# Optimization experiments

Hardware: AMD Instinct MI355X
Metric: run time of the kernel (lower is better)

## Reference

```python
import jax, jax.numpy as jnp
import numpy as np

N, B, S, F_DIM, E = 100000, 4096, 32, 256, 256


def _linear_params(key, fan_in, fan_out):
    kw, kb = jax.random.split(key)
    bound = 1.0 / np.sqrt(fan_in)
    W = jax.random.uniform(kw, (fan_in, fan_out), jnp.float32, -bound, bound)
    b = jax.random.uniform(kb, (fan_out,), jnp.float32, -bound, bound)
    return W, b


def setup_inputs() -> dict:
    key = jax.random.key(0)
    ks = jax.random.split(key, 10)
    Wm, bm = _linear_params(ks[4], F_DIM, E)
    Wq, bq = _linear_params(ks[5], F_DIM, E)
    Wk, bk = _linear_params(ks[6], F_DIM, E)
    Wv, bv = _linear_params(ks[7], F_DIM, E)
    Wc, bc = _linear_params(ks[8], 2 * E, E)
    return {
        "nodes": jax.random.randint(ks[0], (B,), 0, N),
        "neigh_mean": jax.random.randint(ks[1], (B, S), 0, N),
        "neigh_attn": jax.random.randint(ks[2], (B, S), 0, N),
        "id2feat": jax.random.normal(ks[3], (N, F_DIM), jnp.float32),
        "Wm": Wm, "bm": bm,
        "Wq": Wq, "bq": bq,
        "Wk": Wk, "bk": bk,
        "Wv": Wv, "bv": bv,
        "Wc": Wc, "bc": bc,
    }


def reference(nodes, neigh_mean, neigh_attn, id2feat,
              Wm, bm, Wq, bq, Wk, bk, Wv, bv, Wc, bc):
    self_feats = id2feat[nodes]                                   # [B, F]

    # MeanAggregator1: per-row mean of W(id2feat[neighbors]).
    # (mean(W x + b) == W mean(x) + b by linearity; all rows have S neighbors)
    ctx = jnp.mean(id2feat[neigh_mean], axis=1) @ Wm + bm          # [B, E]

    # AttnAggregator1: self-query attention over [neighbors ; self].
    neigh = id2feat[neigh_attn]                                    # [B, S, F]
    cat = jnp.concatenate([neigh, self_feats[:, None, :]], axis=1)  # [B, S+1, F]
    Q = self_feats @ Wq + bq                                       # [B, E]
    K = cat @ Wk + bk                                              # [B, S+1, E]
    V = cat @ Wv + bv                                              # [B, S+1, E]
    scores = jnp.einsum('be,bse->bs', Q, K)                        # [B, S+1]
    # Torch mask loop with uniform neighbor length S masks column S (the self slot)
    pad_mask = jnp.arange(S + 1) >= S                              # [S+1]
    scores = jnp.where(pad_mask[None, :], -jnp.inf, scores)
    attn = jax.nn.softmax(scores, axis=-1)
    mix = jnp.einsum('bs,bse->be', attn, V)                        # [B, E]

    combined = jnp.tanh(jnp.concatenate([mix, ctx], axis=-1) @ Wc + bc)  # [B, E]
    norm = jnp.linalg.norm(combined, axis=-1, keepdims=True)
    return combined / jnp.maximum(norm, 1e-12)                     # F.normalize(p=2)
```

## Files before the change

### kernel.cpp

```cpp
#include <hip/hip_runtime.h>
#include <math.h>

#define S_NEI 32

__global__ __launch_bounds__(256) void transpose256(const float* __restrict__ in,
                                                    float* __restrict__ outT) {
    __shared__ float tile[32][33];
    const int bx = blockIdx.x * 32, by = blockIdx.y * 32;
    const int x = threadIdx.x, y = threadIdx.y;
#pragma unroll
    for (int i = 0; i < 32; i += 8)
        tile[y + i][x] = in[(by + y + i) * 256 + bx + x];
    __syncthreads();
#pragma unroll
    for (int i = 0; i < 32; i += 8)
        outT[(bx + y + i) * 256 + by + x] = tile[x][y + i];
}

template <int KT>
__device__ __forceinline__ void gemm_tile8(const float* __restrict__ A, int row0,
                                           const float* __restrict__ B,
                                           float acc[2][4], float* __restrict__ sA,
                                           float* __restrict__ sB) {
    const int t = threadIdx.x;
    const int tr = t >> 6, tc = t & 63;
    const int r = t >> 5;
    const int k1 = t & 31;
    const size_t arow = (size_t)(row0 + r) * KT;
    for (int kb = 0; kb < KT; kb += 32) {
        sA[k1 * 12 + r] = A[arow + kb + k1];
#pragma unroll
        for (int i = 0; i < 8; ++i) {
            *reinterpret_cast<float4*>(&sB[(i * 4 + tr) * 256 + tc * 4]) =
                *reinterpret_cast<const float4*>(&B[(size_t)(kb + i * 4 + tr) * 256 + tc * 4]);
        }
        __syncthreads();
#pragma unroll
        for (int k = 0; k < 32; ++k) {
            const float2 a2 = *reinterpret_cast<const float2*>(&sA[k * 12 + tr * 2]);
            const float4 b4 = *reinterpret_cast<const float4*>(&sB[k * 256 + tc * 4]);
            acc[0][0] += a2.x * b4.x; acc[0][1] += a2.x * b4.y;
            acc[0][2] += a2.x * b4.z; acc[0][3] += a2.x * b4.w;
            acc[1][0] += a2.y * b4.x; acc[1][1] += a2.y * b4.y;
            acc[1][2] += a2.y * b4.z; acc[1][3] += a2.y * b4.w;
        }
        __syncthreads();
    }
}

__global__ __launch_bounds__(256) void precompute3(const float* __restrict__ Wq,
                                                   const float* __restrict__ Wv,
                                                   const float* __restrict__ Wm,
                                                   const float* __restrict__ Wc,
                                                   const float* __restrict__ WkT,
                                                   float* __restrict__ Wqk,
                                                   float* __restrict__ Wvc,
                                                   float* __restrict__ Wmc) {
    __shared__ float sA[32 * 12];
    __shared__ float sB[32 * 256];
    float acc[2][4] = {};
    const float *Ap, *Bp;
    float* Cp;
    switch (blockIdx.y) {
        case 0: Ap = Wq; Bp = WkT; Cp = Wqk; break;
        case 1: Ap = Wv; Bp = Wc; Cp = Wvc; break;
        default: Ap = Wm; Bp = Wc + 256 * 256; Cp = Wmc; break;
    }
    const int row0 = blockIdx.x * 8;
    gemm_tile8<256>(Ap, row0, Bp, acc, sA, sB);
    const int tr = threadIdx.x >> 6, tc = threadIdx.x & 63;
#pragma unroll
    for (int i = 0; i < 2; ++i) {
        float4 v = make_float4(acc[i][0], acc[i][1], acc[i][2], acc[i][3]);
        *reinterpret_cast<float4*>(&Cp[(row0 + tr * 2 + i) * 256 + tc * 4]) = v;
    }
}

__global__ __launch_bounds__(256) void bias_k(const float* __restrict__ bq,
                                              const float* __restrict__ bv,
                                              const float* __restrict__ bm,
                                              const float* __restrict__ bc,
                                              const float* __restrict__ Wc,
                                              const float* __restrict__ WkT,
                                              float* __restrict__ bqk,
                                              float* __restrict__ bfull) {
    const int c = blockIdx.x;
    const int e = threadIdx.x;
    const int w = e >> 6, l = e & 63;
    float a = bq[e] * WkT[e * 256 + c];
    float v = bv[e] * Wc[e * 256 + c] + bm[e] * Wc[(256 + e) * 256 + c];
    __shared__ float redA[4], redV[4];
#pragma unroll
    for (int off = 32; off; off >>= 1) { a += __shfl_xor(a, off); v += __shfl_xor(v, off); }
    if (l == 0) { redA[w] = a; redV[w] = v; }
    __syncthreads();
    if (e == 0) {
        bqk[c] = redA[0] + redA[1] + redA[2] + redA[3];
        bfull[c] = bc[c] + redV[0] + redV[1] + redV[2] + redV[3];
    }
}

#define FMA8(a0, a1, b4)                                                   \
    do {                                                                   \
        acc[0][0] += (a0).x * (b4).x; acc[0][1] += (a0).x * (b4).y;        \
        acc[0][2] += (a0).x * (b4).z; acc[0][3] += (a0).x * (b4).w;        \
        acc[1][0] += (a0).y * (b4).x; acc[1][1] += (a0).y * (b4).y;        \
        acc[1][2] += (a0).y * (b4).z; acc[1][3] += (a0).y * (b4).w;        \
        acc[2][0] += (a0).z * (b4).x; acc[2][1] += (a0).z * (b4).y;        \
        acc[2][2] += (a0).z * (b4).z; acc[2][3] += (a0).z * (b4).w;        \
        acc[3][0] += (a0).w * (b4).x; acc[3][1] += (a0).w * (b4).y;        \
        acc[3][2] += (a0).w * (b4).z; acc[3][3] += (a0).w * (b4).w;        \
        acc[4][0] += (a1).x * (b4).x; acc[4][1] += (a1).x * (b4).y;        \
        acc[4][2] += (a1).x * (b4).z; acc[4][3] += (a1).x * (b4).w;        \
        acc[5][0] += (a1).y * (b4).x; acc[5][1] += (a1).y * (b4).y;        \
        acc[5][2] += (a1).y * (b4).z; acc[5][3] += (a1).y * (b4).w;        \
        acc[6][0] += (a1).z * (b4).x; acc[6][1] += (a1).z * (b4).y;        \
        acc[6][2] += (a1).z * (b4).z; acc[6][3] += (a1).z * (b4).w;        \
        acc[7][0] += (a1).w * (b4).x; acc[7][1] += (a1).w * (b4).y;        \
        acc[7][2] += (a1).w * (b4).z; acc[7][3] += (a1).w * (b4).w;        \
    } while (0)

__global__ __launch_bounds__(256, 2) void fused8(const float* __restrict__ id2feat,
                                                 const int* __restrict__ nodes,
                                                 const int* __restrict__ neigh_mean,
                                                 const int* __restrict__ neigh_attn,
                                                 const float* __restrict__ Wqk,
                                                 const float* __restrict__ bqk,
                                                 const float* __restrict__ Wfused,
                                                 const float* __restrict__ bfull,
                                                 float* __restrict__ out) {
    __shared__ __align__(16) char smem[59904];
    float* sA  = (float*)smem;
    float* sAF = (float*)smem;
    float* sP  = (float*)(smem + 24576);
    float* sQk = (float*)(smem + 49536);
    int*   sIA = (int*)(smem + 57856);
    int*   sIM = (int*)(smem + 58880);

    const int t = threadIdx.x;
    const int w = t >> 6, l = t & 63;
    const int col4 = l * 4;
    const int row0 = blockIdx.x * 8;

    sIA[t] = neigh_attn[(size_t)row0 * S_NEI + t];
    sIM[t] = neigh_mean[(size_t)row0 * S_NEI + t];

    {
        const int r = t & 7;
        const int k0 = (t >> 3) * 8;
        const size_t arow = (size_t)nodes[row0 + r] * 256;
#pragma unroll
        for (int u = 0; u < 2; ++u) {
            const float4 v = *reinterpret_cast<const float4*>(&id2feat[arow + k0 + u * 4]);
            sA[(k0 + u * 4 + 0) * 12 + r] = v.x;
            sA[(k0 + u * 4 + 1) * 12 + r] = v.y;
            sA[(k0 + u * 4 + 2) * 12 + r] = v.z;
            sA[(k0 + u * 4 + 3) * 12 + r] = v.w;
        }
    }
    __syncthreads();

    float acc[8][4] = {};

    {
        const int kbeg = w * 64;
        const float* Bp = Wqk + (size_t)kbeg * 256 + col4;
        float4 bufA[8], bufB[8];
#pragma unroll
        for (int j = 0; j < 8; ++j)
            bufA[j] = *reinterpret_cast<const float4*>(&Bp[(size_t)j * 256]);
        for (int kb = 0; kb < 64; kb += 16) {
#pragma unroll
            for (int j = 0; j < 8; ++j)
                bufB[j] = *reinterpret_cast<const float4*>(&Bp[(size_t)(kb + 8 + j) * 256]);
#pragma unroll
            for (int j = 0; j < 8; ++j) {
                const int k = kbeg + kb + j;
                const float4 a0 = *reinterpret_cast<const float4*>(&sA[k * 12]);
                const float4 a1 = *reinterpret_cast<const float4*>(&sA[k * 12 + 4]);
                FMA8(a0, a1, bufA[j]);
            }
            if (kb + 16 < 64) {
#pragma unroll
                for (int j = 0; j < 8; ++j)
                    bufA[j] = *reinterpret_cast<const float4*>(&Bp[(size_t)(kb + 16 + j) * 256]);
            }
#pragma unroll
            for (int j = 0; j < 8; ++j) {
                const int k = kbeg + kb + 8 + j;
                const float4 a0 = *reinterpret_cast<const float4*>(&sA[k * 12]);
                const float4 a1 = *reinterpret_cast<const float4*>(&sA[k * 12 + 4]);
                FMA8(a0, a1, bufB[j]);
            }
        }
    }
    if (w > 0) {
#pragma unroll
        for (int i = 0; i < 8; ++i)
            *reinterpret_cast<float4*>(&sP[(w - 1) * 2080 + i * 260 + col4]) =
                make_float4(acc[i][0], acc[i][1], acc[i][2], acc[i][3]);
    }
    __syncthreads();
    if (w == 0) {
        const float4 bq4 = *reinterpret_cast<const float4*>(&bqk[col4]);
#pragma unroll
        for (int i = 0; i < 8; ++i) {
            float4 v = make_float4(acc[i][0] + bq4.x, acc[i][1] + bq4.y,
                                   acc[i][2] + bq4.z, acc[i][3] + bq4.w);
#pragma unroll
            for (int pw = 0; pw < 3; ++pw) {
                const float4 p =
                    *reinterpret_cast<const float4*>(&sP[pw * 2080 + i * 260 + col4]);
                v.x += p.x; v.y += p.y; v.z += p.z; v.w += p.w;
            }
            *reinterpret_cast<float4*>(&sQk[i * 260 + col4]) = v;
        }
    }
    __syncthreads();

    const float4* f4 = reinterpret_cast<const float4*>(id2feat);
#pragma unroll
    for (int bb = 0; bb < 2; ++bb) {
        const int b = w * 2 + bb;
        float4 r[32];
#pragma unroll
        for (int j = 0; j < 32; ++j) r[j] = f4[(size_t)sIA[b * 32 + j] * 64 + l];
        float4 macc = make_float4(0.f, 0.f, 0.f, 0.f);
#pragma unroll
        for (int j = 0; j < 32; ++j) {
            const float4 v = f4[(size_t)sIM[b * 32 + j] * 64 + l];
            macc.x += v.x; macc.y += v.y; macc.z += v.z; macc.w += v.w;
        }
        const float4 q = *reinterpret_cast<const float4*>(&sQk[b * 260 + col4]);
        float sc[32];
#pragma unroll
        for (int j = 0; j < 32; ++j) {
            float p = q.x * r[j].x + q.y * r[j].y + q.z * r[j].z + q.w * r[j].w;
#pragma unroll
            for (int off = 32; off; off >>= 1) p += __shfl_xor(p, off);
            sc[j] = p;
        }
        float m = sc[0];
#pragma unroll
        for (int j = 1; j < 32; ++j) m = fmaxf(m, sc[j]);
        float sum = 0.f;
#pragma unroll
        for (int j = 0; j < 32; ++j) sum += __expf(sc[j] - m);
        const float inv = 1.0f / sum;
        float4 wa = make_float4(0.f, 0.f, 0.f, 0.f);
#pragma unroll
        for (int j = 0; j < 32; ++j) {
            const float wg = __expf(sc[j] - m);
            wa.x += wg * r[j].x; wa.y += wg * r[j].y;
            wa.z += wg * r[j].z; wa.w += wg * r[j].w;
        }
        const float mixv[4] = {wa.x * inv, wa.y * inv, wa.z * inv, wa.w * inv};
        const float mev[4] = {macc.x * (1.f / 32), macc.y * (1.f / 32),
                              macc.z * (1.f / 32), macc.w * (1.f / 32)};
#pragma unroll
        for (int c = 0; c < 4; ++c) {
            sAF[(col4 + c) * 12 + b] = mixv[c];
            sAF[(256 + col4 + c) * 12 + b] = mev[c];
        }
    }
    __syncthreads();

#pragma unroll
    for (int i = 0; i < 8; ++i)
#pragma unroll
        for (int c = 0; c < 4; ++c) acc[i][c] = 0.f;
    {
        const int kbeg = w * 128;
        const float* Bp = Wfused + (size_t)kbeg * 256 + col4;
        float4 bufA[8], bufB[8];
#pragma unroll
        for (int j = 0; j < 8; ++j)
            bufA[j] = *reinterpret_cast<const float4*>(&Bp[(size_t)j * 256]);
        for (int kb = 0; kb < 128; kb += 16) {
#pragma unroll
            for (int j = 0; j < 8; ++j)
                bufB[j] = *reinterpret_cast<const float4*>(&Bp[(size_t)(kb + 8 + j) * 256]);
#pragma unroll
            for (int j = 0; j < 8; ++j) {
                const int k = kbeg + kb + j;
                const float4 a0 = *reinterpret_cast<const float4*>(&sAF[k * 12]);
                const float4 a1 = *reinterpret_cast<const float4*>(&sAF[k * 12 + 4]);
                FMA8(a0, a1, bufA[j]);
            }
            if (kb + 16 < 128) {
#pragma unroll
                for (int j = 0; j < 8; ++j)
                    bufA[j] = *reinterpret_cast<const float4*>(&Bp[(size_t)(kb + 16 + j) * 256]);
            }
#pragma unroll
            for (int j = 0; j < 8; ++j) {
                const int k = kbeg + kb + 8 + j;
                const float4 a0 = *reinterpret_cast<const float4*>(&sAF[k * 12]);
                const float4 a1 = *reinterpret_cast<const float4*>(&sAF[k * 12 + 4]);
                FMA8(a0, a1, bufB[j]);
            }
        }
    }
    if (w > 0) {
#pragma unroll
        for (int i = 0; i < 8; ++i)
            *reinterpret_cast<float4*>(&sP[(w - 1) * 2080 + i * 260 + col4]) =
                make_float4(acc[i][0], acc[i][1], acc[i][2], acc[i][3]);
    }
    __syncthreads();
    if (w == 0) {
        const float4 bf4 = *reinterpret_cast<const float4*>(&bfull[col4]);
#pragma unroll
        for (int i = 0; i < 8; ++i) {
            float v0 = acc[i][0] + bf4.x;
            float v1 = acc[i][1] + bf4.y;
            float v2 = acc[i][2] + bf4.z;
            float v3 = acc[i][3] + bf4.w;
#pragma unroll
            for (int pw = 0; pw < 3; ++pw) {
                const float4 p =
                    *reinterpret_cast<const float4*>(&sP[pw * 2080 + i * 260 + col4]);
                v0 += p.x; v1 += p.y; v2 += p.z; v3 += p.w;
            }
            v0 = tanhf(v0); v1 = tanhf(v1); v2 = tanhf(v2); v3 = tanhf(v3);
            float pw2 = v0 * v0 + v1 * v1 + v2 * v2 + v3 * v3;
#pragma unroll
            for (int off = 32; off; off >>= 1) pw2 += __shfl_xor(pw2, off);
            const float invn = 1.0f / fmaxf(sqrtf(pw2), 1e-12f);
            *reinterpret_cast<float4*>(&out[(size_t)(row0 + i) * 256 + col4]) =
                make_float4(v0 * invn, v1 * invn, v2 * invn, v3 * invn);
        }
    }
}

extern "C" void kernel_launch(void* const* d_in, const int* in_sizes, int n_in,
                              void* d_out, int out_size, void* d_ws, size_t ws_size,
                              hipStream_t stream) {
    const int* nodes      = (const int*)d_in[0];
    const int* neigh_mean = (const int*)d_in[1];
    const int* neigh_attn = (const int*)d_in[2];
    const float* id2feat  = (const float*)d_in[3];
    const float* Wm = (const float*)d_in[4];
    const float* bm = (const float*)d_in[5];
    const float* Wq = (const float*)d_in[6];
    const float* bq = (const float*)d_in[7];
    const float* Wk = (const float*)d_in[8];
    const float* Wv = (const float*)d_in[10];
    const float* bv = (const float*)d_in[11];
    const float* Wc = (const float*)d_in[12];
    const float* bc = (const float*)d_in[13];
    float* out = (float*)d_out;

    const int B = in_sizes[0];

    float* ws    = (float*)d_ws;
    float* WkT   = ws;
    float* Wqk   = ws + 65536;
    float* Wvc   = ws + 131072;
    float* Wmc   = ws + 196608;
    float* bqk   = ws + 262144;
    float* bfull = ws + 262400;

    transpose256<<<dim3(8, 8), dim3(32, 8), 0, stream>>>(Wk, WkT);
    precompute3<<<dim3(32, 3), 256, 0, stream>>>(Wq, Wv, Wm, Wc, WkT, Wqk, Wvc, Wmc);
    bias_k<<<256, 256, 0, stream>>>(bq, bv, bm, bc, Wc, WkT, bqk, bfull);
    fused8<<<B / 8, 256, 0, stream>>>(id2feat, nodes, neigh_mean, neigh_attn,
                                      Wqk, bqk, Wvc , bfull, out);
}
```

Before: 94.00 us.

## Double block to 512 threads, split GEMM columns, one row per wave in attention

The fused kernel now runs 512 threads per block. The GEMMs split output columns into two halves of 2 columns per lane, with a 4-way K split reduced through shared memory. Attention assigns one batch row per wave and processes neighbors in two chunks of 16 with an online-softmax merge, which lowers register pressure from holding 32 float4s. Shared memory shrinks and is reused, with a padded A layout meant to cut bank conflicts. The aims are more resident waves to hide gather latency and better occupancy, at the cost of extra syncs and a cross-wave norm reduction.

```diff
diff --git a/kernel.cpp b/kernel.cpp
--- a/kernel.cpp
+++ b/kernel.cpp
@@ -100,27 +100,22 @@
     }
 }
 
-#define FMA8(a0, a1, b4)                                                   \
-    do {                                                                   \
-        acc[0][0] += (a0).x * (b4).x; acc[0][1] += (a0).x * (b4).y;        \
-        acc[0][2] += (a0).x * (b4).z; acc[0][3] += (a0).x * (b4).w;        \
-        acc[1][0] += (a0).y * (b4).x; acc[1][1] += (a0).y * (b4).y;        \
-        acc[1][2] += (a0).y * (b4).z; acc[1][3] += (a0).y * (b4).w;        \
-        acc[2][0] += (a0).z * (b4).x; acc[2][1] += (a0).z * (b4).y;        \
-        acc[2][2] += (a0).z * (b4).z; acc[2][3] += (a0).z * (b4).w;        \
-        acc[3][0] += (a0).w * (b4).x; acc[3][1] += (a0).w * (b4).y;        \
-        acc[3][2] += (a0).w * (b4).z; acc[3][3] += (a0).w * (b4).w;        \
-        acc[4][0] += (a1).x * (b4).x; acc[4][1] += (a1).x * (b4).y;        \
-        acc[4][2] += (a1).x * (b4).z; acc[4][3] += (a1).x * (b4).w;        \
-        acc[5][0] += (a1).y * (b4).x; acc[5][1] += (a1).y * (b4).y;        \
-        acc[5][2] += (a1).y * (b4).z; acc[5][3] += (a1).y * (b4).w;        \
-        acc[6][0] += (a1).z * (b4).x; acc[6][1] += (a1).z * (b4).y;        \
-        acc[6][2] += (a1).z * (b4).z; acc[6][3] += (a1).z * (b4).w;        \
-        acc[7][0] += (a1).w * (b4).x; acc[7][1] += (a1).w * (b4).y;        \
-        acc[7][2] += (a1).w * (b4).z; acc[7][3] += (a1).w * (b4).w;        \
+
+#define SAF(k) ((k) * 12 + (((k) >> 3) << 2))
+
+#define FMAB(a0, a1, b2)                                                    \
+    do {                                                                    \
+        acc[0][0] += (a0).x * (b2).x; acc[0][1] += (a0).x * (b2).y;         \
+        acc[1][0] += (a0).y * (b2).x; acc[1][1] += (a0).y * (b2).y;         \
+        acc[2][0] += (a0).z * (b2).x; acc[2][1] += (a0).z * (b2).y;         \
+        acc[3][0] += (a0).w * (b2).x; acc[3][1] += (a0).w * (b2).y;         \
+        acc[4][0] += (a1).x * (b2).x; acc[4][1] += (a1).x * (b2).y;         \
+        acc[5][0] += (a1).y * (b2).x; acc[5][1] += (a1).y * (b2).y;         \
+        acc[6][0] += (a1).z * (b2).x; acc[6][1] += (a1).z * (b2).y;         \
+        acc[7][0] += (a1).w * (b2).x; acc[7][1] += (a1).w * (b2).y;         \
     } while (0)
 
-__global__ __launch_bounds__(256, 2) void fused8(const float* __restrict__ id2feat,
+__global__ __launch_bounds__(512, 4) void fused8(const float* __restrict__ id2feat,
                                                  const int* __restrict__ nodes,
                                                  const int* __restrict__ neigh_mean,
                                                  const int* __restrict__ neigh_attn,
@@ -129,206 +124,226 @@
                                                  const float* __restrict__ Wfused,
                                                  const float* __restrict__ bfull,
                                                  float* __restrict__ out) {
-    __shared__ __align__(16) char smem[59904];
-    float* sA  = (float*)smem;
-    float* sAF = (float*)smem;
-    float* sP  = (float*)(smem + 24576);
-    float* sQk = (float*)(smem + 49536);
-    int*   sIA = (int*)(smem + 57856);
-    int*   sIM = (int*)(smem + 58880);
+    __shared__ __align__(16) char smem[36224];
+    float* R0  = (float*)smem;
+    float* sQk = (float*)(smem + 25600);
+    int*   sIA = (int*)(smem + 33920);
+    int*   sIM = (int*)(smem + 34944);
+    float* sN  = (float*)(smem + 35968);
 
     const int t = threadIdx.x;
     const int w = t >> 6, l = t & 63;
-    const int col4 = l * 4;
+    const int kq = w & 3, ch = w >> 2;
+    const int c2 = ch * 128 + l * 2;
     const int row0 = blockIdx.x * 8;
 
-    sIA[t] = neigh_attn[(size_t)row0 * S_NEI + t];
-    sIM[t] = neigh_mean[(size_t)row0 * S_NEI + t];
+    if (t < 256) sIA[t] = neigh_attn[(size_t)row0 * S_NEI + t];
+    else sIM[t - 256] = neigh_mean[(size_t)row0 * S_NEI + (t - 256)];
 
     {
         const int r = t & 7;
-        const int k0 = (t >> 3) * 8;
-        const size_t arow = (size_t)nodes[row0 + r] * 256;
-#pragma unroll
-        for (int u = 0; u < 2; ++u) {
-            const float4 v = *reinterpret_cast<const float4*>(&id2feat[arow + k0 + u * 4]);
-            sA[(k0 + u * 4 + 0) * 12 + r] = v.x;
-            sA[(k0 + u * 4 + 1) * 12 + r] = v.y;
-            sA[(k0 + u * 4 + 2) * 12 + r] = v.z;
-            sA[(k0 + u * 4 + 3) * 12 + r] = v.w;
-        }
-    }
-    __syncthreads();
-
-    float acc[8][4] = {};
+        const int k0 = (t >> 3) * 4;
+        const float4 v = *reinterpret_cast<const float4*>(
+            &id2feat[(size_t)nodes[row0 + r] * 256 + k0]);
+        R0[SAF(k0 + 0) + r] = v.x;
+        R0[SAF(k0 + 1) + r] = v.y;
+        R0[SAF(k0 + 2) + r] = v.z;
+        R0[SAF(k0 + 3) + r] = v.w;
+    }
+    __syncthreads();
+
+    float acc[8][2] = {};
 
     {
-        const int kbeg = w * 64;
-        const float* Bp = Wqk + (size_t)kbeg * 256 + col4;
-        float4 bufA[8], bufB[8];
+        const float* Bp = Wqk + (size_t)(kq * 64) * 256 + c2;
+        float2 bufA[8], bufB[8];
 #pragma unroll
         for (int j = 0; j < 8; ++j)
-            bufA[j] = *reinterpret_cast<const float4*>(&Bp[(size_t)j * 256]);
+            bufA[j] = *reinterpret_cast<const float2*>(&Bp[(size_t)j * 256]);
         for (int kb = 0; kb < 64; kb += 16) {
 #pragma unroll
             for (int j = 0; j < 8; ++j)
-                bufB[j] = *reinterpret_cast<const float4*>(&Bp[(size_t)(kb + 8 + j) * 256]);
+                bufB[j] = *reinterpret_cast<const float2*>(&Bp[(size_t)(kb + 8 + j) * 256]);
 #pragma unroll
             for (int j = 0; j < 8; ++j) {
-                const int k = kbeg + kb + j;
-                const float4 a0 = *reinterpret_cast<const float4*>(&sA[k * 12]);
-                const float4 a1 = *reinterpret_cast<const float4*>(&sA[k * 12 + 4]);
-                FMA8(a0, a1, bufA[j]);
+                const int k = kq * 64 + kb + j;
+                const float4 a0 = *reinterpret_cast<const float4*>(&R0[SAF(k)]);
+                const float4 a1 = *reinterpret_cast<const float4*>(&R0[SAF(k) + 4]);
+                FMAB(a0, a1, bufA[j]);
             }
             if (kb + 16 < 64) {
 #pragma unroll
                 for (int j = 0; j < 8; ++j)
-                    bufA[j] = *reinterpret_cast<const float4*>(&Bp[(size_t)(kb + 16 + j) * 256]);
+                    bufA[j] = *reinterpret_cast<const float2*>(&Bp[(size_t)(kb + 16 + j) * 256]);
             }
 #pragma unroll
             for (int j = 0; j < 8; ++j) {
-                const int k = kbeg + kb + 8 + j;
-                const float4 a0 = *reinterpret_cast<const float4*>(&sA[k * 12]);
-                const float4 a1 = *reinterpret_cast<const float4*>(&sA[k * 12 + 4]);
-                FMA8(a0, a1, bufB[j]);
-            }
-        }
-    }
-    if (w > 0) {
-#pragma unroll
-        for (int i = 0; i < 8; ++i)
-            *reinterpret_cast<float4*>(&sP[(w - 1) * 2080 + i * 260 + col4]) =
-                make_float4(acc[i][0], acc[i][1], acc[i][2], acc[i][3]);
-    }
-    __syncthreads();
-    if (w == 0) {
-        const float4 bq4 = *reinterpret_cast<const float4*>(&bqk[col4]);
-#pragma unroll
-        for (int i = 0; i < 8; ++i) {
-            float4 v = make_float4(acc[i][0] + bq4.x, acc[i][1] + bq4.y,
-                                   acc[i][2] + bq4.z, acc[i][3] + bq4.w);
-#pragma unroll
-            for (int pw = 0; pw < 3; ++pw) {
-                const float4 p =
-                    *reinterpret_cast<const float4*>(&sP[pw * 2080 + i * 260 + col4]);
-                v.x += p.x; v.y += p.y; v.z += p.z; v.w += p.w;
-            }
-            *reinterpret_cast<float4*>(&sQk[i * 260 + col4]) = v;
-        }
-    }
-    __syncthreads();
-
-    const float4* f4 = reinterpret_cast<const float4*>(id2feat);
-#pragma unroll
-    for (int bb = 0; bb < 2; ++bb) {
-        const int b = w * 2 + bb;
-        float4 r[32];
-#pragma unroll
-        for (int j = 0; j < 32; ++j) r[j] = f4[(size_t)sIA[b * 32 + j] * 64 + l];
+                const int k = kq * 64 + kb + 8 + j;
+                const float4 a0 = *reinterpret_cast<const float4*>(&R0[SAF(k)]);
+                const float4 a1 = *reinterpret_cast<const float4*>(&R0[SAF(k) + 4]);
+                FMAB(a0, a1, bufB[j]);
+            }
+        }
+    }
+    __syncthreads();
+    if (kq) {
+        float* p = R0 + ((ch * 3 + (kq - 1)) * 8) * 132 + l * 2;
+#pragma unroll
+        for (int r = 0; r < 8; ++r) {
+            p[r * 132 + 0] = acc[r][0];
+            p[r * 132 + 1] = acc[r][1];
+        }
+    }
+    __syncthreads();
+    if (kq == 0) {
+#pragma unroll
+        for (int r = 0; r < 8; ++r) {
+            float v0 = acc[r][0] + bqk[c2 + 0];
+            float v1 = acc[r][1] + bqk[c2 + 1];
+#pragma unroll
+            for (int s = 0; s < 3; ++s) {
+                const float* p = R0 + ((ch * 3 + s) * 8 + r) * 132 + l * 2;
+                v0 += p[0]; v1 += p[1];
+            }
+            sQk[r * 260 + c2 + 0] = v0;
+            sQk[r * 260 + c2 + 1] = v1;
+        }
+    }
+    __syncthreads();
+
+    {
+        const int b = w;
+        const float4 q = *reinterpret_cast<const float4*>(&sQk[b * 260 + 4 * l]);
+        const float4* f4 = reinterpret_cast<const float4*>(id2feat);
+        const int* ia = sIA + b * 32;
+        const int* im = sIM + b * 32;
         float4 macc = make_float4(0.f, 0.f, 0.f, 0.f);
-#pragma unroll
-        for (int j = 0; j < 32; ++j) {
-            const float4 v = f4[(size_t)sIM[b * 32 + j] * 64 + l];
-            macc.x += v.x; macc.y += v.y; macc.z += v.z; macc.w += v.w;
-        }
-        const float4 q = *reinterpret_cast<const float4*>(&sQk[b * 260 + col4]);
-        float sc[32];
-#pragma unroll
-        for (int j = 0; j < 32; ++j) {
-            float p = q.x * r[j].x + q.y * r[j].y + q.z * r[j].z + q.w * r[j].w;
-#pragma unroll
-            for (int off = 32; off; off >>= 1) p += __shfl_xor(p, off);
-            sc[j] = p;
-        }
-        float m = sc[0];
-#pragma unroll
-        for (int j = 1; j < 32; ++j) m = fmaxf(m, sc[j]);
-        float sum = 0.f;
-#pragma unroll
-        for (int j = 0; j < 32; ++j) sum += __expf(sc[j] - m);
-        const float inv = 1.0f / sum;
-        float4 wa = make_float4(0.f, 0.f, 0.f, 0.f);
-#pragma unroll
-        for (int j = 0; j < 32; ++j) {
-            const float wg = __expf(sc[j] - m);
-            wa.x += wg * r[j].x; wa.y += wg * r[j].y;
-            wa.z += wg * r[j].z; wa.w += wg * r[j].w;
-        }
-        const float mixv[4] = {wa.x * inv, wa.y * inv, wa.z * inv, wa.w * inv};
+        float mch[2], ech[2];
+        float4 wch[2];
+#pragma unroll
+        for (int cch = 0; cch < 2; ++cch) {
+            float4 r[16];
+#pragma unroll
+            for (int j = 0; j < 16; ++j) r[j] = f4[(size_t)ia[cch * 16 + j] * 64 + l];
+#pragma unroll
+            for (int j = 0; j < 16; ++j) {
+                const float4 v = f4[(size_t)im[cch * 16 + j] * 64 + l];
+                macc.x += v.x; macc.y += v.y; macc.z += v.z; macc.w += v.w;
+            }
+            float p[16];
+#pragma unroll
+            for (int j = 0; j < 16; ++j) {
+                float s = q.x * r[j].x + q.y * r[j].y + q.z * r[j].z + q.w * r[j].w;
+#pragma unroll
+                for (int off = 32; off; off >>= 1) s += __shfl_xor(s, off);
+                p[j] = s;
+            }
+            float m = p[0];
+#pragma unroll
+            for (int j = 1; j < 16; ++j) m = fmaxf(m, p[j]);
+            float e = 0.f;
+            float4 wa = make_float4(0.f, 0.f, 0.f, 0.f);
+#pragma unroll
+            for (int j = 0; j < 16; ++j) {
+                const float g = __expf(p[j] - m);
+                e += g;
+                wa.x += g * r[j].x; wa.y += g * r[j].y;
+                wa.z += g * r[j].z; wa.w += g * r[j].w;
+            }
+            mch[cch] = m; ech[cch] = e; wch[cch] = wa;
+        }
+        const float m = fmaxf(mch[0], mch[1]);
+        const float f0 = __expf(mch[0] - m), f1 = __expf(mch[1] - m);
+        const float inv = 1.0f / (ech[0] * f0 + ech[1] * f1);
+        const float mix[4] = {(wch[0].x * f0 + wch[1].x * f1) * inv,
+                              (wch[0].y * f0 + wch[1].y * f1) * inv,
+                              (wch[0].z * f0 + wch[1].z * f1) * inv,
+                              (wch[0].w * f0 + wch[1].w * f1) * inv};
         const float mev[4] = {macc.x * (1.f / 32), macc.y * (1.f / 32),
                               macc.z * (1.f / 32), macc.w * (1.f / 32)};
 #pragma unroll
         for (int c = 0; c < 4; ++c) {
-            sAF[(col4 + c) * 12 + b] = mixv[c];
-            sAF[(256 + col4 + c) * 12 + b] = mev[c];
-        }
-    }
-    __syncthreads();
-
-#pragma unroll
-    for (int i = 0; i < 8; ++i)
-#pragma unroll
-        for (int c = 0; c < 4; ++c) acc[i][c] = 0.f;
+            R0[SAF(4 * l + c) + b] = mix[c];
+            R0[SAF(256 + 4 * l + c) + b] = mev[c];
+        }
+    }
+    __syncthreads();
+
+#pragma unroll
+    for (int r = 0; r < 8; ++r) { acc[r][0] = 0.f; acc[r][1] = 0.f; }
     {
-        const int kbeg = w * 128;
-        const float* Bp = Wfused + (size_t)kbeg * 256 + col4;
-        float4 bufA[8], bufB[8];
+        const float* Bp = Wfused + (size_t)(kq * 128) * 256 + c2;
+        float2 bufA[8], bufB[8];
 #pragma unroll
         for (int j = 0; j < 8; ++j)
-            bufA[j] = *reinterpret_cast<const float4*>(&Bp[(size_t)j * 256]);
+            bufA[j] = *reinterpret_cast<const float2*>(&Bp[(size_t)j * 256]);
         for (int kb = 0; kb < 128; kb += 16) {
 #pragma unroll
             for (int j = 0; j < 8; ++j)
-                bufB[j] = *reinterpret_cast<const float4*>(&Bp[(size_t)(kb + 8 + j) * 256]);
+                bufB[j] = *reinterpret_cast<const float2*>(&Bp[(size_t)(kb + 8 + j) * 256]);
 #pragma unroll
             for (int j = 0; j < 8; ++j) {
-                const int k = kbeg + kb + j;
-                const float4 a0 = *reinterpret_cast<const float4*>(&sAF[k * 12]);
-                const float4 a1 = *reinterpret_cast<const float4*>(&sAF[k * 12 + 4]);
-                FMA8(a0, a1, bufA[j]);
+                const int k = kq * 128 + kb + j;
+                const float4 a0 = *reinterpret_cast<const float4*>(&R0[SAF(k)]);
+                const float4 a1 = *reinterpret_cast<const float4*>(&R0[SAF(k) + 4]);
+                FMAB(a0, a1, bufA[j]);
             }
             if (kb + 16 < 128) {
 #pragma unroll
                 for (int j = 0; j < 8; ++j)
-                    bufA[j] = *reinterpret_cast<const float4*>(&Bp[(size_t)(kb + 16 + j) * 256]);
+                    bufA[j] = *reinterpret_cast<const float2*>(&Bp[(size_t)(kb + 16 + j) * 256]);
             }
 #pragma unroll
             for (int j = 0; j < 8; ++j) {
-                const int k = kbeg + kb + 8 + j;
-                const float4 a0 = *reinterpret_cast<const float4*>(&sAF[k * 12]);
-                const float4 a1 = *reinterpret_cast<const float4*>(&sAF[k * 12 + 4]);
-                FMA8(a0, a1, bufB[j]);
-            }
-        }
-    }
-    if (w > 0) {
-#pragma unroll
-        for (int i = 0; i < 8; ++i)
-            *reinterpret_cast<float4*>(&sP[(w - 1) * 2080 + i * 260 + col4]) =
-                make_float4(acc[i][0], acc[i][1], acc[i][2], acc[i][3]);
-    }
-    __syncthreads();
-    if (w == 0) {
-        const float4 bf4 = *reinterpret_cast<const float4*>(&bfull[col4]);
-#pragma unroll
-        for (int i = 0; i < 8; ++i) {
-            float v0 = acc[i][0] + bf4.x;
-            float v1 = acc[i][1] + bf4.y;
-            float v2 = acc[i][2] + bf4.z;
-            float v3 = acc[i][3] + bf4.w;
-#pragma unroll
-            for (int pw = 0; pw < 3; ++pw) {
-                const float4 p =
-                    *reinterpret_cast<const float4*>(&sP[pw * 2080 + i * 260 + col4]);
-                v0 += p.x; v1 += p.y; v2 += p.z; v3 += p.w;
-            }
-            v0 = tanhf(v0); v1 = tanhf(v1); v2 = tanhf(v2); v3 = tanhf(v3);
-            float pw2 = v0 * v0 + v1 * v1 + v2 * v2 + v3 * v3;
-#pragma unroll
-            for (int off = 32; off; off >>= 1) pw2 += __shfl_xor(pw2, off);
-            const float invn = 1.0f / fmaxf(sqrtf(pw2), 1e-12f);
-            *reinterpret_cast<float4*>(&out[(size_t)(row0 + i) * 256 + col4]) =
-                make_float4(v0 * invn, v1 * invn, v2 * invn, v3 * invn);
+                const int k = kq * 128 + kb + 8 + j;
+                const float4 a0 = *reinterpret_cast<const float4*>(&R0[SAF(k)]);
+                const float4 a1 = *reinterpret_cast<const float4*>(&R0[SAF(k) + 4]);
+                FMAB(a0, a1, bufB[j]);
+            }
+        }
+    }
+    __syncthreads();
+    if (kq) {
+        float* p = R0 + ((ch * 3 + (kq - 1)) * 8) * 132 + l * 2;
+#pragma unroll
+        for (int r = 0; r < 8; ++r) {
+            p[r * 132 + 0] = acc[r][0];
+            p[r * 132 + 1] = acc[r][1];
+        }
+    }
+    __syncthreads();
+    float v[8][2];
+    if (kq == 0) {
+#pragma unroll
+        for (int r = 0; r < 8; ++r) {
+            float v0 = acc[r][0] + bfull[c2 + 0];
+            float v1 = acc[r][1] + bfull[c2 + 1];
+#pragma unroll
+            for (int s = 0; s < 3; ++s) {
+                const float* p = R0 + ((ch * 3 + s) * 8 + r) * 132 + l * 2;
+                v0 += p[0]; v1 += p[1];
+            }
+            v[r][0] = tanhf(v0);
+            v[r][1] = tanhf(v1);
+        }
+        float sq[8];
+#pragma unroll
+        for (int r = 0; r < 8; ++r) {
+            float s = v[r][0] * v[r][0] + v[r][1] * v[r][1];
+#pragma unroll
+            for (int off = 32; off; off >>= 1) s += __shfl_xor(s, off);
+            sq[r] = s;
+        }
+        if (l < 8) sN[ch * 8 + l] = sq[l];
+    }
+    __syncthreads();
+    if (kq == 0) {
+#pragma unroll
+        for (int r = 0; r < 8; ++r) {
+            const float S = sN[r] + sN[8 + r];
+            const float invn = 1.0f / fmaxf(sqrtf(S), 1e-12f);
+            *reinterpret_cast<float2*>(&out[(size_t)(row0 + r) * 256 + c2]) =
+                make_float2(v[r][0] * invn, v[r][1] * invn);
         }
     }
 }
@@ -364,6 +379,6 @@
     transpose256<<<dim3(8, 8), dim3(32, 8), 0, stream>>>(Wk, WkT);
     precompute3<<<dim3(32, 3), 256, 0, stream>>>(Wq, Wv, Wm, Wc, WkT, Wqk, Wvc, Wmc);
     bias_k<<<256, 256, 0, stream>>>(bq, bv, bm, bc, Wc, WkT, bqk, bfull);
-    fused8<<<B / 8, 256, 0, stream>>>(id2feat, nodes, neigh_mean, neigh_attn,
+    fused8<<<B / 8, 512, 0, stream>>>(id2feat, nodes, neigh_mean, neigh_attn,
                                       Wqk, bqk, Wvc , bfull, out);
 }
```

Measured after the change: 134.6 us. 43.2% more time.
